# Performance work log

Hardware: AMD Instinct MI355X
Metric: run time of the kernel (lower is better)

The kernel has to match this reference:

```python
import jax, jax.numpy as jnp
import numpy as np
import math

DIM = 1024
HEADS = 16
HEAD_DIM = DIM // HEADS
FFN = 4096
B, S = 2, 2048
EPS = 1e-12


def layernorm(x, w, b):
    u = jnp.mean(x, axis=-1, keepdims=True)
    s = jnp.mean((x - u) ** 2, axis=-1, keepdims=True)
    return w * ((x - u) / jnp.sqrt(s + EPS)) + b


def setup_inputs() -> dict:
    key = jax.random.key(0)
    ks = jax.random.split(key, 8)
    scale = 0.02
    return {
        "x": jax.random.normal(ks[0], (B, S, DIM), dtype=jnp.float32),
        "mask": jnp.zeros((1, 1, S, S), dtype=jnp.float32),
        "wq": jax.random.normal(ks[1], (DIM, DIM), dtype=jnp.float32) * scale,
        "wk": jax.random.normal(ks[2], (DIM, DIM), dtype=jnp.float32) * scale,
        "wv": jax.random.normal(ks[3], (DIM, DIM), dtype=jnp.float32) * scale,
        "wo": jax.random.normal(ks[4], (DIM, DIM), dtype=jnp.float32) * scale,
        "w1": jax.random.normal(ks[5], (DIM, FFN), dtype=jnp.float32) * scale,
        "w2": jax.random.normal(ks[6], (FFN, DIM), dtype=jnp.float32) * scale,
        "ln1_w": jnp.ones((DIM,), dtype=jnp.float32),
        "ln1_b": jnp.zeros((DIM,), dtype=jnp.float32),
        "ln2_w": jnp.ones((DIM,), dtype=jnp.float32),
        "ln2_b": jnp.zeros((DIM,), dtype=jnp.float32),
    }


def reference(x, mask, wq, wk, wv, wo, w1, w2, ln1_w, ln1_b, ln2_w, ln2_b):
    # --- attention sub-block (pre-LN) ---
    h = layernorm(x, ln1_w, ln1_b)
    q = (h @ wq).reshape(B, S, HEADS, HEAD_DIM).transpose(0, 2, 1, 3)  # [B,H,S,D]
    k = (h @ wk).reshape(B, S, HEADS, HEAD_DIM).transpose(0, 2, 1, 3)
    v = (h @ wv).reshape(B, S, HEADS, HEAD_DIM).transpose(0, 2, 1, 3)
    scores = jnp.einsum("bhsd,bhtd->bhst", q, k) / math.sqrt(HEAD_DIM)
    scores = scores + mask
    probs = jax.nn.softmax(scores.astype(jnp.float32), axis=-1).astype(q.dtype)
    attn = jnp.einsum("bhst,bhtd->bhsd", probs, v)  # [B,H,S,D]
    attn = attn.transpose(0, 2, 1, 3).reshape(B, S, DIM)
    x = x + attn @ wo
    # --- FFN sub-block (pre-LN) ---
    h = layernorm(x, ln2_w, ln2_b)
    m = jax.nn.gelu(h @ w1, approximate=False) @ w2
    return x + m
```

## Files before the change

### kernel.cpp

```cpp
#include <hip/hip_runtime.h>
#include <math.h>


#define DIMSZ 1024
#define SEQ   2048
#define BATCH 2
#define NHEAD 16
#define HD    64
#define FFNSZ 4096
#define ROWS  (BATCH*SEQ)
#define KSPLIT 2
#define KRANGE (SEQ/KSPLIT)

typedef __attribute__((ext_vector_type(8))) short bf8_t;
typedef __attribute__((ext_vector_type(4))) float f4_t;

__device__ __forceinline__ unsigned short f2bf(float f) {
  union { float f; unsigned u; } c; c.f = f;
  unsigned u = c.u;
  return (unsigned short)((u + 0x7fffu + ((u >> 16) & 1u)) >> 16);
}

__device__ __forceinline__ float bf2f(unsigned short u) {
  union { unsigned u; float f; } c; c.u = ((unsigned)u) << 16; return c.f;
}

__device__ __forceinline__ float fast_exp2(float x) {
#if __has_builtin(__builtin_amdgcn_exp2f)
  return __builtin_amdgcn_exp2f(x);
#else
  return exp2f(x);
#endif
}

__device__ __forceinline__ unsigned int pk_trunc_bf16(float a, float b) {
#if __has_builtin(__builtin_amdgcn_perm)
  return __builtin_amdgcn_perm(__float_as_uint(b), __float_as_uint(a), 0x07060302u);
#else
  return (__float_as_uint(b) & 0xffff0000u) | (__float_as_uint(a) >> 16);
#endif
}

__device__ __forceinline__ void async16(const void* g, void* l) {
  __builtin_amdgcn_global_load_lds((const __attribute__((address_space(1))) void*)g,
                                   (__attribute__((address_space(3))) void*)l,
                                   16, 0, 0);
}

__device__ __forceinline__ f4_t mfma_bf16(bf8_t a, bf8_t b, f4_t c) {
  return __builtin_amdgcn_mfma_f32_16x16x32_bf16(a, b, c, 0, 0, 0);
}

__global__ __launch_bounds__(256) void ln_kernel(const float* __restrict__ x,
                                                 const float* __restrict__ w,
                                                 const float* __restrict__ b,
                                                 unsigned short* __restrict__ out) {
  int row  = blockIdx.x * 4 + (threadIdx.x >> 6);
  int lane = threadIdx.x & 63;
  const float4* xr = (const float4*)(x + (size_t)row * DIMSZ);
  float4 v[4];
  float s = 0.f, s2 = 0.f;
#pragma unroll
  for (int i = 0; i < 4; ++i) {
    v[i] = xr[lane + 64*i];
    s  += (v[i].x + v[i].y) + (v[i].z + v[i].w);
    s2 += (v[i].x*v[i].x + v[i].y*v[i].y) + (v[i].z*v[i].z + v[i].w*v[i].w);
  }
#pragma unroll
  for (int off = 32; off; off >>= 1) {
    s  += __shfl_xor(s,  off);
    s2 += __shfl_xor(s2, off);
  }
  float mean = s * (1.f/DIMSZ);
  float var  = s2 * (1.f/DIMSZ) - mean*mean;
  float rstd = rsqrtf(var + 1e-12f);
  const float4* wr = (const float4*)w;
  const float4* br = (const float4*)b;
#pragma unroll
  for (int i = 0; i < 4; ++i) {
    float4 wv = wr[lane + 64*i];
    float4 bv = br[lane + 64*i];
    ushort4 o;
    o.x = f2bf((v[i].x - mean) * rstd * wv.x + bv.x);
    o.y = f2bf((v[i].y - mean) * rstd * wv.y + bv.y);
    o.z = f2bf((v[i].z - mean) * rstd * wv.z + bv.z);
    o.w = f2bf((v[i].w - mean) * rstd * wv.w + bv.w);
    *(ushort4*)(out + (size_t)row * DIMSZ + (size_t)(lane + 64*i) * 4) = o;
  }
}

__global__ __launch_bounds__(256) void wtrans4_kernel(const float* __restrict__ w0,
                                                      const float* __restrict__ w1,
                                                      const float* __restrict__ w2,
                                                      const float* __restrict__ w3,
                                                      unsigned short* __restrict__ o0,
                                                      unsigned short* __restrict__ o1,
                                                      unsigned short* __restrict__ o2,
                                                      unsigned short* __restrict__ o3) {
  const int K = 1024, N = 1024;
  const float* w = (blockIdx.z == 0) ? w0 : (blockIdx.z == 1) ? w1 : (blockIdx.z == 2) ? w2 : w3;
  unsigned short* wT = (blockIdx.z == 0) ? o0 : (blockIdx.z == 1) ? o1 : (blockIdx.z == 2) ? o2 : o3;
  __shared__ float t[32][33];
  int tx = threadIdx.x & 31, ty = threadIdx.x >> 5;
  int n0 = blockIdx.x * 32, k0 = blockIdx.y * 32;
#pragma unroll
  for (int i = 0; i < 4; ++i)
    t[ty + 8*i][tx] = w[(size_t)(k0 + ty + 8*i) * N + n0 + tx];
  __syncthreads();
#pragma unroll
  for (int i = 0; i < 4; ++i)
    wT[(size_t)(n0 + ty + 8*i) * K + k0 + tx] = f2bf(t[tx][ty + 8*i]);
}

__global__ __launch_bounds__(256) void wtrans_kernel(const float* __restrict__ w,
                                                     unsigned short* __restrict__ wT,
                                                     int K, int N) {
  __shared__ float t[32][33];
  int tx = threadIdx.x & 31, ty = threadIdx.x >> 5;
  int n0 = blockIdx.x * 32, k0 = blockIdx.y * 32;
#pragma unroll
  for (int i = 0; i < 4; ++i)
    t[ty + 8*i][tx] = w[(size_t)(k0 + ty + 8*i) * N + n0 + tx];
  __syncthreads();
#pragma unroll
  for (int i = 0; i < 4; ++i)
    wT[(size_t)(n0 + ty + 8*i) * K + k0 + tx] = f2bf(t[tx][ty + 8*i]);
}

__global__ __launch_bounds__(256) void vt_kernel(const unsigned short* __restrict__ qkv,
                                                 unsigned short* __restrict__ vt) {
  __shared__ unsigned short tile[64][65];
  int bh = blockIdx.y, b = bh >> 4, h = bh & 15;
  int s0 = blockIdx.x * 64;
  int tx = threadIdx.x & 63, ty = threadIdx.x >> 6;
#pragma unroll
  for (int i = 0; i < 16; ++i) {
    int s = ty + i*4;
    tile[s][tx] = qkv[((size_t)(b*SEQ) + s0 + s) * 3072 + 2048 + h*HD + tx];
  }
  __syncthreads();
#pragma unroll
  for (int i = 0; i < 16; ++i) {
    int d = ty + i*4;
    vt[((size_t)bh * HD + d) * SEQ + s0 + tx] = tile[tx][d];
  }
}

template<int EPI, int NT>
__global__ __launch_bounds__(256) void gemm_bt(const unsigned short* __restrict__ A,
                                               const unsigned short* __restrict__ Bt,
                                               void* __restrict__ Cv,
                                               const float* __restrict__ res,
                                               int M, int N, int K) {
  constexpr int JT = NT / 32;
  __shared__ unsigned short As[2][128][32];
  __shared__ unsigned short Bs[2][NT][32];
  int tid  = threadIdx.x;
  int wv   = tid >> 6, lane = tid & 63, quad = lane >> 4, ml = lane & 15;
  int wrow = (wv >> 1) * 64, wcol = (wv & 1) * (NT/2);
  const unsigned short* Ab = A  + (size_t)blockIdx.y * 128 * K;
  const unsigned short* Bb = Bt + (size_t)blockIdx.x * NT  * K;

  f4_t acc[4][JT];
#pragma unroll
  for (int i = 0; i < 4; ++i)
#pragma unroll
    for (int j = 0; j < JT; ++j) acc[i][j] = (f4_t){0.f, 0.f, 0.f, 0.f};

  int r0 = tid >> 2, c0 = (tid & 3) * 8;

  for (int k0 = 0; k0 < K; k0 += 64) {
#pragma unroll
    for (int h = 0; h < 2; ++h) {
      const unsigned short* ap = Ab + (size_t)r0 * K + k0 + h*32 + c0;
      async16(ap,          &As[h][r0][c0]);
      async16(ap + 64*K,   &As[h][r0 + 64][c0]);
      const unsigned short* bp = Bb + (size_t)r0 * K + k0 + h*32 + c0;
      async16(bp,          &Bs[h][r0][c0]);
      if constexpr (NT == 128)
        async16(bp + 64*K, &Bs[h][r0 + 64][c0]);
    }
    __syncthreads();

#pragma unroll
    for (int h = 0; h < 2; ++h) {
      bf8_t af[4], bfr[JT];
#pragma unroll
      for (int i = 0; i < 4; ++i)
        af[i] = *(const bf8_t*)(&As[h][wrow + i*16 + ml][quad * 8]);
#pragma unroll
      for (int j = 0; j < JT; ++j)
        bfr[j] = *(const bf8_t*)(&Bs[h][wcol + j*16 + ml][quad * 8]);
#pragma unroll
      for (int i = 0; i < 4; ++i)
#pragma unroll
        for (int j = 0; j < JT; ++j)
          acc[i][j] = mfma_bf16(bfr[j], af[i], acc[i][j]);
    }
    __syncthreads();
  }

#pragma unroll
  for (int i = 0; i < 4; ++i) {
    int m = blockIdx.y * 128 + wrow + i*16 + ml;
#pragma unroll
    for (int j = 0; j < JT; ++j) {
      int n = blockIdx.x * NT + wcol + j*16 + quad*4;
      size_t off = (size_t)m * N + n;
      if constexpr (EPI == 2) {
        float4 rv = *(const float4*)(res + off);
        float4 ov;
        ov.x = rv.x + acc[i][j][0];
        ov.y = rv.y + acc[i][j][1];
        ov.z = rv.z + acc[i][j][2];
        ov.w = rv.w + acc[i][j][3];
        *(float4*)((float*)Cv + off) = ov;
      } else {
        float v0 = acc[i][j][0], v1 = acc[i][j][1], v2 = acc[i][j][2], v3 = acc[i][j][3];
        if constexpr (EPI == 1) {
          v0 = 0.5f * v0 * (1.f + erff(v0 * 0.70710678118654752f));
          v1 = 0.5f * v1 * (1.f + erff(v1 * 0.70710678118654752f));
          v2 = 0.5f * v2 * (1.f + erff(v2 * 0.70710678118654752f));
          v3 = 0.5f * v3 * (1.f + erff(v3 * 0.70710678118654752f));
        }
        ushort4 o;
        o.x = f2bf(v0); o.y = f2bf(v1); o.z = f2bf(v2); o.w = f2bf(v3);
        *(ushort4*)((unsigned short*)Cv + off) = o;
      }
    }
  }
}

__global__ __launch_bounds__(256) void attn_part(const unsigned short* __restrict__ qkv,
                                                 const unsigned short* __restrict__ vt,
                                                 const float* __restrict__ mask,
                                                 unsigned short* __restrict__ pbuf,
                                                 float* __restrict__ lbuf) {
  __shared__ unsigned short Ks[2][64][32];
  __shared__ unsigned short Vs[2][64][32];
  __shared__ unsigned short Ps[4][2][16][72];

  int kz = blockIdx.y;
  int bh = blockIdx.z, b = bh >> 4, h = bh & 15;
  int tid = threadIdx.x;
  int wv = tid >> 6, lane = tid & 63;
  int quad = lane >> 4, ml = lane & 15;
  int q0 = blockIdx.x * 128;
  int qA = q0 + wv * 32 + ml;
  int qB = qA + 16;
  int kbeg = kz * KRANGE;

  const unsigned short* qrowA = qkv + ((size_t)(b*SEQ) + qA) * 3072 + h*HD;
  const unsigned short* qrowB = qkv + ((size_t)(b*SEQ) + qB) * 3072 + h*HD;
  bf8_t qf[2][2];
  qf[0][0] = *(const bf8_t*)(qrowA + quad*8);
  qf[0][1] = *(const bf8_t*)(qrowA + 32 + quad*8);
  qf[1][0] = *(const bf8_t*)(qrowB + quad*8);
  qf[1][1] = *(const bf8_t*)(qrowB + 32 + quad*8);

  const unsigned short* kbase = qkv + ((size_t)(b*SEQ) + kbeg) * 3072 + DIMSZ + h*HD;
  const unsigned short* vbase = vt + (size_t)bh * HD * SEQ + kbeg;
  const float* mrowA = mask + (size_t)qA * SEQ + kbeg;
  const float* mrowB = mask + (size_t)qB * SEQ + kbeg;

  int srow = tid >> 2;
  int scol = (tid & 3) * 8;

  f4_t O[2][4];
#pragma unroll
  for (int g = 0; g < 2; ++g)
#pragma unroll
    for (int dt = 0; dt < 4; ++dt) O[g][dt] = (f4_t){0.f, 0.f, 0.f, 0.f};
  float lR[2] = {0.f, 0.f};

  const float C1 = 0.18033688011112042f;
  const float C2 = 1.4426950408889634f;

  for (int t0 = 0; t0 < KRANGE; t0 += 64) {
    float4 mvA[4], mvB[4];
#pragma unroll
    for (int mt = 0; mt < 4; ++mt) {
      mvA[mt] = *(const float4*)(mrowA + t0 + mt*16 + quad*4);
      mvB[mt] = *(const float4*)(mrowB + t0 + mt*16 + quad*4);
    }

    __syncthreads();
#pragma unroll
    for (int dh = 0; dh < 2; ++dh)
      async16(kbase + (size_t)(t0 + srow) * 3072 + dh*32 + scol,
              &Ks[dh][0][0] + (size_t)tid * 8);
#pragma unroll
    for (int kc = 0; kc < 2; ++kc)
      async16(vbase + (size_t)srow * SEQ + t0 + kc*32 + scol,
              &Vs[kc][0][0] + (size_t)tid * 8);
    __syncthreads();

#pragma unroll
    for (int mt = 0; mt < 4; ++mt) {
      bf8_t kf0 = *(const bf8_t*)(&Ks[0][mt*16 + ml][quad*8]);
      bf8_t kf1 = *(const bf8_t*)(&Ks[1][mt*16 + ml][quad*8]);
#pragma unroll
      for (int g = 0; g < 2; ++g) {
        f4_t s = (f4_t){0.f, 0.f, 0.f, 0.f};
        s = mfma_bf16(kf0, qf[g][0], s);
        s = mfma_bf16(kf1, qf[g][1], s);
        const float4& mv = g ? mvB[mt] : mvA[mt];
        float p0 = fast_exp2(fmaf(s[0], C1, mv.x * C2));
        float p1 = fast_exp2(fmaf(s[1], C1, mv.y * C2));
        float p2 = fast_exp2(fmaf(s[2], C1, mv.z * C2));
        float p3 = fast_exp2(fmaf(s[3], C1, mv.w * C2));
        lR[g] += (p0 + p1) + (p2 + p3);
        uint2 pk;
        pk.x = pk_trunc_bf16(p0, p1);
        pk.y = pk_trunc_bf16(p2, p3);
        *(uint2*)(&Ps[wv][g][ml][mt*16 + quad*4]) = pk;
      }
    }

#pragma unroll
    for (int kc = 0; kc < 2; ++kc) {
      bf8_t pfA = *(const bf8_t*)(&Ps[wv][0][ml][kc*32 + quad*8]);
      bf8_t pfB = *(const bf8_t*)(&Ps[wv][1][ml][kc*32 + quad*8]);
#pragma unroll
      for (int dt = 0; dt < 4; ++dt) {
        bf8_t vf = *(const bf8_t*)(&Vs[kc][dt*16 + ml][quad*8]);
        O[0][dt] = mfma_bf16(vf, pfA, O[0][dt]);
        O[1][dt] = mfma_bf16(vf, pfB, O[1][dt]);
      }
    }
  }

#pragma unroll
  for (int g = 0; g < 2; ++g) {
    lR[g] += __shfl_xor(lR[g], 16);
    lR[g] += __shfl_xor(lR[g], 32);
    int q = g ? qB : qA;
    size_t pb = ((size_t)(bh * KSPLIT + kz) * SEQ + q) * HD;
#pragma unroll
    for (int dt = 0; dt < 4; ++dt) {
      ushort4 o;
      o.x = f2bf(O[g][dt][0]);
      o.y = f2bf(O[g][dt][1]);
      o.z = f2bf(O[g][dt][2]);
      o.w = f2bf(O[g][dt][3]);
      *(ushort4*)(pbuf + pb + dt*16 + quad*4) = o;
    }
    if (quad == 0)
      lbuf[(size_t)(bh * KSPLIT + kz) * SEQ + q] = lR[g];
  }
}

__global__ __launch_bounds__(256) void attn_combine(const unsigned short* __restrict__ pbuf,
                                                    const float* __restrict__ lbuf,
                                                    unsigned short* __restrict__ attno) {
  int t = blockIdx.x * 256 + threadIdx.x;
  int dchunk = t & 15;
  int q = (t >> 4) & (SEQ - 1);
  int bh = t >> 15;
  int b = bh >> 4, h = bh & 15;
  size_t o0 = ((size_t)(bh * KSPLIT + 0) * SEQ + q) * HD + dchunk * 4;
  size_t o1 = ((size_t)(bh * KSPLIT + 1) * SEQ + q) * HD + dchunk * 4;
  ushort4 a = *(const ushort4*)(pbuf + o0);
  ushort4 c = *(const ushort4*)(pbuf + o1);
  float l = lbuf[(size_t)(bh * KSPLIT + 0) * SEQ + q]
          + lbuf[(size_t)(bh * KSPLIT + 1) * SEQ + q];
  float inv = 1.f / l;
  ushort4 o;
  o.x = f2bf((bf2f(a.x) + bf2f(c.x)) * inv);
  o.y = f2bf((bf2f(a.y) + bf2f(c.y)) * inv);
  o.z = f2bf((bf2f(a.z) + bf2f(c.z)) * inv);
  o.w = f2bf((bf2f(a.w) + bf2f(c.w)) * inv);
  *(ushort4*)(attno + ((size_t)(b*SEQ) + q) * DIMSZ + h*HD + dchunk*4) = o;
}

extern "C" void kernel_launch(void* const* d_in, const int* in_sizes, int n_in,
                              void* d_out, int out_size, void* d_ws, size_t ws_size,
                              hipStream_t stream) {
  const float* x    = (const float*)d_in[0];
  const float* mask = (const float*)d_in[1];
  const float* wq   = (const float*)d_in[2];
  const float* wk   = (const float*)d_in[3];
  const float* wvp  = (const float*)d_in[4];
  const float* wo   = (const float*)d_in[5];
  const float* w1   = (const float*)d_in[6];
  const float* w2   = (const float*)d_in[7];
  const float* ln1w = (const float*)d_in[8];
  const float* ln1b = (const float*)d_in[9];
  const float* ln2w = (const float*)d_in[10];
  const float* ln2b = (const float*)d_in[11];
  float* out = (float*)d_out;

  char* ws = (char*)d_ws;
  unsigned short* wqkvT  = (unsigned short*)(ws + 0);
  unsigned short* woT    = (unsigned short*)(ws + 6291456);
  unsigned short* w1T    = (unsigned short*)(ws + 8388608);
  unsigned short* w2T    = (unsigned short*)(ws + 16777216);
  unsigned short* attno  = (unsigned short*)(ws + 25165824);
  float*          x2     = (float*)         (ws + 33554432);
  unsigned short* hbuf   = (unsigned short*)(ws + 50331648);
  unsigned short* qkvb   = (unsigned short*)(ws + 58720256);
  unsigned short* vtb    = (unsigned short*)(ws + 83886080);
  unsigned short* gbuf   = (unsigned short*)(ws + 58720256);
  unsigned short* pbuf   = (unsigned short*)(ws + 33554432);
  float*          lbuf   = (float*)         (ws + 50331648);

  ln_kernel<<<ROWS/4, 256, 0, stream>>>(x, ln1w, ln1b, hbuf);
  wtrans4_kernel<<<dim3(32, 32, 4), 256, 0, stream>>>(wq, wk, wvp, wo,
      wqkvT, wqkvT + 1024*1024, wqkvT + 2*1024*1024, woT);
  wtrans_kernel<<<dim3(128, 32), 256, 0, stream>>>(w1, w1T, 1024, 4096);
  wtrans_kernel<<<dim3(32, 128), 256, 0, stream>>>(w2, w2T, 4096, 1024);
  gemm_bt<0,128><<<dim3(3072/128, 4096/128), 256, 0, stream>>>(hbuf, wqkvT, qkvb, nullptr, ROWS, 3072, 1024);
  vt_kernel<<<dim3(SEQ/64, BATCH*NHEAD), 256, 0, stream>>>(qkvb, vtb);
  attn_part<<<dim3(SEQ/128, KSPLIT, BATCH*NHEAD), 256, 0, stream>>>(qkvb, vtb, mask, pbuf, lbuf);
  attn_combine<<<(BATCH*NHEAD*SEQ*(HD/4))/256, 256, 0, stream>>>(pbuf, lbuf, attno);
  gemm_bt<2,64><<<dim3(1024/64, 4096/128), 256, 0, stream>>>(attno, woT, x2, x, ROWS, 1024, 1024);
  ln_kernel<<<ROWS/4, 256, 0, stream>>>(x2, ln2w, ln2b, hbuf);
  gemm_bt<1,128><<<dim3(4096/128, 4096/128), 256, 0, stream>>>(hbuf, w1T, gbuf, nullptr, ROWS, FFNSZ, 1024);
  gemm_bt<2,64><<<dim3(1024/64, 4096/128), 256, 0, stream>>>(gbuf, w2T, out, x2, ROWS, 1024, 4096);

  (void)in_sizes; (void)n_in; (void)out_size; (void)ws_size;
}
```

Baseline: 411.8 us.

## Overlap LDS staging with MFMA compute in GEMM and attention; cheaper GELU

The GEMM main loop now splits each K-tile into two halves and prefetches one half into LDS while the MFMAs run on the other. The attention loop likewise alternates between K and V tile loads and the QK/PV compute, and prefetches mask rows one tile ahead. Both changes aim to hide global-to-LDS latency that the old load-then-sync-then-compute structure exposed. The erff-based GELU epilogue is replaced with an Abramowitz-Stegun polynomial that uses hardware rcp and exp2. This adds small approximation error and keeps more mask registers live.

```diff
diff --git a/kernel.cpp b/kernel.cpp
--- a/kernel.cpp
+++ b/kernel.cpp
@@ -31,6 +31,28 @@
 #else
   return exp2f(x);
 #endif
+}
+
+__device__ __forceinline__ float fast_rcp(float x) {
+#if __has_builtin(__builtin_amdgcn_rcpf)
+  return __builtin_amdgcn_rcpf(x);
+#else
+  return 1.f / x;
+#endif
+}
+
+__device__ __forceinline__ float gelu_fast(float x) {
+  float ax = fabsf(x) * 0.70710678118654752f;
+  float t  = fast_rcp(fmaf(0.3275911f, ax, 1.f));
+  float p  = fmaf(t, 1.061405429f, -1.453152027f);
+  p = fmaf(t, p, 1.421413741f);
+  p = fmaf(t, p, -0.284496736f);
+  p = fmaf(t, p, 0.254829592f);
+  p = p * t;
+  float e  = fast_exp2(-ax * ax * 1.4426950408889634f);
+  float er = fmaf(-p, e, 1.f);
+  er = copysignf(er, x);
+  return 0.5f * x * (1.f + er);
 }
 
 __device__ __forceinline__ unsigned int pk_trunc_bf16(float a, float b) {
@@ -169,35 +191,38 @@
 
   int r0 = tid >> 2, c0 = (tid & 3) * 8;
 
+  auto stageh = [&](int h, int k0) {
+    const unsigned short* ap = Ab + (size_t)r0 * K + k0 + h*32 + c0;
+    async16(ap,        &As[h][r0][c0]);
+    async16(ap + 64*K, &As[h][r0 + 64][c0]);
+    const unsigned short* bp = Bb + (size_t)r0 * K + k0 + h*32 + c0;
+    async16(bp,        &Bs[h][r0][c0]);
+    if constexpr (NT == 128)
+      async16(bp + 64*K, &Bs[h][r0 + 64][c0]);
+  };
+  auto computeh = [&](int h) {
+    bf8_t af[4], bfr[JT];
+#pragma unroll
+    for (int i = 0; i < 4; ++i)
+      af[i] = *(const bf8_t*)(&As[h][wrow + i*16 + ml][quad * 8]);
+#pragma unroll
+    for (int j = 0; j < JT; ++j)
+      bfr[j] = *(const bf8_t*)(&Bs[h][wcol + j*16 + ml][quad * 8]);
+#pragma unroll
+    for (int i = 0; i < 4; ++i)
+#pragma unroll
+      for (int j = 0; j < JT; ++j)
+        acc[i][j] = mfma_bf16(bfr[j], af[i], acc[i][j]);
+  };
+
+  stageh(0, 0);
   for (int k0 = 0; k0 < K; k0 += 64) {
-#pragma unroll
-    for (int h = 0; h < 2; ++h) {
-      const unsigned short* ap = Ab + (size_t)r0 * K + k0 + h*32 + c0;
-      async16(ap,          &As[h][r0][c0]);
-      async16(ap + 64*K,   &As[h][r0 + 64][c0]);
-      const unsigned short* bp = Bb + (size_t)r0 * K + k0 + h*32 + c0;
-      async16(bp,          &Bs[h][r0][c0]);
-      if constexpr (NT == 128)
-        async16(bp + 64*K, &Bs[h][r0 + 64][c0]);
-    }
-    __syncthreads();
-
-#pragma unroll
-    for (int h = 0; h < 2; ++h) {
-      bf8_t af[4], bfr[JT];
-#pragma unroll
-      for (int i = 0; i < 4; ++i)
-        af[i] = *(const bf8_t*)(&As[h][wrow + i*16 + ml][quad * 8]);
-#pragma unroll
-      for (int j = 0; j < JT; ++j)
-        bfr[j] = *(const bf8_t*)(&Bs[h][wcol + j*16 + ml][quad * 8]);
-#pragma unroll
-      for (int i = 0; i < 4; ++i)
-#pragma unroll
-        for (int j = 0; j < JT; ++j)
-          acc[i][j] = mfma_bf16(bfr[j], af[i], acc[i][j]);
-    }
-    __syncthreads();
+    __syncthreads();
+    stageh(1, k0);
+    computeh(0);
+    __syncthreads();
+    if (k0 + 64 < K) stageh(0, k0 + 64);
+    computeh(1);
   }
 
 #pragma unroll
@@ -218,10 +243,8 @@
       } else {
         float v0 = acc[i][j][0], v1 = acc[i][j][1], v2 = acc[i][j][2], v3 = acc[i][j][3];
         if constexpr (EPI == 1) {
-          v0 = 0.5f * v0 * (1.f + erff(v0 * 0.70710678118654752f));
-          v1 = 0.5f * v1 * (1.f + erff(v1 * 0.70710678118654752f));
-          v2 = 0.5f * v2 * (1.f + erff(v2 * 0.70710678118654752f));
-          v3 = 0.5f * v3 * (1.f + erff(v3 * 0.70710678118654752f));
+          v0 = gelu_fast(v0); v1 = gelu_fast(v1);
+          v2 = gelu_fast(v2); v3 = gelu_fast(v3);
         }
         ushort4 o;
         o.x = f2bf(v0); o.y = f2bf(v1); o.z = f2bf(v2); o.w = f2bf(v3);
@@ -276,25 +299,26 @@
   const float C1 = 0.18033688011112042f;
   const float C2 = 1.4426950408889634f;
 
-  for (int t0 = 0; t0 < KRANGE; t0 += 64) {
-    float4 mvA[4], mvB[4];
-#pragma unroll
-    for (int mt = 0; mt < 4; ++mt) {
-      mvA[mt] = *(const float4*)(mrowA + t0 + mt*16 + quad*4);
-      mvB[mt] = *(const float4*)(mrowB + t0 + mt*16 + quad*4);
-    }
-
-    __syncthreads();
+  auto stageK = [&](int t0) {
 #pragma unroll
     for (int dh = 0; dh < 2; ++dh)
       async16(kbase + (size_t)(t0 + srow) * 3072 + dh*32 + scol,
               &Ks[dh][0][0] + (size_t)tid * 8);
+  };
+  auto stageV = [&](int t0) {
 #pragma unroll
     for (int kc = 0; kc < 2; ++kc)
       async16(vbase + (size_t)srow * SEQ + t0 + kc*32 + scol,
               &Vs[kc][0][0] + (size_t)tid * 8);
-    __syncthreads();
-
+  };
+  auto loadmask = [&](int t0, float4* mA, float4* mB) {
+#pragma unroll
+    for (int mt = 0; mt < 4; ++mt) {
+      mA[mt] = *(const float4*)(mrowA + t0 + mt*16 + quad*4);
+      mB[mt] = *(const float4*)(mrowB + t0 + mt*16 + quad*4);
+    }
+  };
+  auto qk = [&](const float4* mA, const float4* mB) {
 #pragma unroll
     for (int mt = 0; mt < 4; ++mt) {
       bf8_t kf0 = *(const bf8_t*)(&Ks[0][mt*16 + ml][quad*8]);
@@ -304,7 +328,7 @@
         f4_t s = (f4_t){0.f, 0.f, 0.f, 0.f};
         s = mfma_bf16(kf0, qf[g][0], s);
         s = mfma_bf16(kf1, qf[g][1], s);
-        const float4& mv = g ? mvB[mt] : mvA[mt];
+        const float4& mv = g ? mB[mt] : mA[mt];
         float p0 = fast_exp2(fmaf(s[0], C1, mv.x * C2));
         float p1 = fast_exp2(fmaf(s[1], C1, mv.y * C2));
         float p2 = fast_exp2(fmaf(s[2], C1, mv.z * C2));
@@ -316,7 +340,8 @@
         *(uint2*)(&Ps[wv][g][ml][mt*16 + quad*4]) = pk;
       }
     }
-
+  };
+  auto pv = [&]() {
 #pragma unroll
     for (int kc = 0; kc < 2; ++kc) {
       bf8_t pfA = *(const bf8_t*)(&Ps[wv][0][ml][kc*32 + quad*8]);
@@ -328,6 +353,31 @@
         O[1][dt] = mfma_bf16(vf, pfB, O[1][dt]);
       }
     }
+  };
+
+  float4 m0A[4], m0B[4], m1A[4], m1B[4];
+  stageK(0);
+  loadmask(0, m0A, m0B);
+
+#pragma unroll 1
+  for (int c = 0; c < KRANGE/64; c += 2) {
+    int t0 = c*64, t1 = t0 + 64, t2 = t0 + 128;
+    __syncthreads();
+    stageV(t0);
+    qk(m0A, m0B);
+    __syncthreads();
+    stageK(t1);
+    loadmask(t1, m1A, m1B);
+    pv();
+    __syncthreads();
+    stageV(t1);
+    qk(m1A, m1B);
+    __syncthreads();
+    if (t2 < KRANGE) {
+      stageK(t2);
+      loadmask(t2, m0A, m0B);
+    }
+    pv();
   }
 
 #pragma unroll
```

Measured after the change: 425.8 us. +3.4%, slower.
